# Performance work log

Measured on AMD Instinct MI355X. Metric: run time of the kernel, lower is better.

## Reference

```python
import jax, jax.numpy as jnp
import numpy as np

SIM_THRESHOLD = 0.9


def setup_inputs() -> dict:
    key = jax.random.key(0)
    k1, k2 = jax.random.split(key)
    # patches: b * c * num * ws * ws  (b=2, c=8, num=1024, ws=3) -> n = 16384
    patches = jax.random.normal(k1, (2, 8, 1024, 3, 3), dtype=jnp.float32)
    # db: m * ws * ws
    db = jax.random.normal(k2, (16384, 3, 3), dtype=jnp.float32)
    return {"patches": patches, "db": db}


def reference(patches, db):
    ws = patches.shape[-1]
    p = patches.reshape(-1, ws, ws)          # [n, ws, ws]
    n = p.shape[0]
    m = db.shape[0]
    pf = p.reshape(n, -1)                    # [n, ws*ws]
    df = db.reshape(m, -1)                   # [m, ws*ws]
    dot = pf @ df.T                          # [n, m], tiny K=ws*ws -> memory bound
    norm_n = jnp.linalg.norm(pf, axis=1, keepdims=True)   # [n, 1]
    norm_m = jnp.linalg.norm(df, axis=1, keepdims=True)   # [m, 1]
    cos = dot / (norm_n * norm_m.T)          # [n, m] cosine similarity
    # patch kept only if dissimilar to EVERY db entry
    mask = jnp.all(cos < SIM_THRESHOLD, axis=1)            # [n] bool
    # jit-friendly fixed-shape compaction: zero out rejected patches instead of
    # dropping rows (original does db = cat(db, patches[mask]))
    filtered = jnp.where(mask[:, None, None], p, jnp.zeros((), p.dtype))
    return jnp.concatenate([db.reshape(-1, ws, ws), filtered], axis=0)  # [m+n, ws, ws]
```

## Files before the change

### kernel.cpp

```cpp
#include <hip/hip_runtime.h>

#define NPATCH 16384
#define NDB    16384
#define WS9    9
#define KP     16
#define JCH    32
#define CHUNK  (NDB / JCH)
#define TILES  (CHUNK / 32)
#define BAND_LO 0.89998f
#define BAND_HI 0.90002f
#define COPY_BLOCKS 144

typedef short bf16x8 __attribute__((ext_vector_type(8)));
typedef float f32x16 __attribute__((ext_vector_type(16)));

#define MAX3(a,b,c) fmaxf(fmaxf((a),(b)),(c))

__device__ __forceinline__ float np_norm9(const float* v) {
#pragma clang fp contract(off)
    float q0 = v[0] * v[0], q1 = v[1] * v[1], q2 = v[2] * v[2], q3 = v[3] * v[3];
    float q4 = v[4] * v[4], q5 = v[5] * v[5], q6 = v[6] * v[6], q7 = v[7] * v[7];
    float q8 = v[8] * v[8];
    float s = ((q0 + q1) + (q2 + q3)) + ((q4 + q5) + (q6 + q7));
    s = s + q8;
    return sqrtf(s);
}

__device__ __forceinline__ unsigned short f2bf(float x) {
    unsigned u = __float_as_uint(x);
    return (unsigned short)((u + 0x7fffu + ((u >> 16) & 1u)) >> 16);
}
__device__ __forceinline__ float bf2f(unsigned short h) {
    return __uint_as_float(((unsigned)h) << 16);
}

__device__ __forceinline__ void stage_row(const float* __restrict__ src,
                                          unsigned short* dh, unsigned short* dl) {
    float v[WS9];
#pragma unroll
    for (int k = 0; k < WS9; k++) v[k] = src[k];
    float inv = 1.0f / np_norm9(v);
    unsigned short h[KP], l[KP];
#pragma unroll
    for (int k = 0; k < KP; k++) {
        float x = (k < WS9) ? v[k] * inv : 0.0f;
        h[k] = f2bf(x);
        l[k] = f2bf(x - bf2f(h[k]));
    }
    int hw[8], lw[8];
#pragma unroll
    for (int k = 0; k < 8; k++) {
        hw[k] = (int)h[2 * k] | ((int)h[2 * k + 1] << 16);
        lw[k] = (int)l[2 * k] | ((int)l[2 * k + 1] << 16);
    }
    ((int4*)dh)[0] = make_int4(hw[0], hw[1], hw[2], hw[3]);
    ((int4*)dh)[1] = make_int4(hw[4], hw[5], hw[6], hw[7]);
    ((int4*)dl)[0] = make_int4(lw[0], lw[1], lw[2], lw[3]);
    ((int4*)dl)[1] = make_int4(lw[4], lw[5], lw[6], lw[7]);
}

__global__ __launch_bounds__(256) void k_phase1(const float* __restrict__ patches,
                                                const float* __restrict__ db,
                                                float* __restrict__ partial) {
    __shared__ __align__(16) unsigned short s_dnh[CHUNK * KP];
    __shared__ __align__(16) unsigned short s_dnl[CHUNK * KP];
    __shared__ __align__(16) unsigned short s_pnh[256 * KP];
    __shared__ __align__(16) unsigned short s_pnl[256 * KP];

    int jbase = blockIdx.y * CHUNK;
    int ibase = blockIdx.x * 256;
#pragma unroll
    for (int rr = 0; rr < CHUNK / 256; rr++) {
        int r = rr * 256 + threadIdx.x;
        stage_row(db + (size_t)(jbase + r) * WS9, &s_dnh[r * KP], &s_dnl[r * KP]);
    }
    stage_row(patches + (size_t)(ibase + threadIdx.x) * WS9,
              &s_pnh[threadIdx.x * KP], &s_pnl[threadIdx.x * KP]);
    __syncthreads();

    int lane = threadIdx.x & 63;
    int wave = threadIdx.x >> 6;
    int col = lane & 31;
    int half = lane >> 5;
    int i0 = ibase + wave * 64;

    const bf16x8* Ph = (const bf16x8*)s_pnh;
    const bf16x8* Pl = (const bf16x8*)s_pnl;
    bf16x8 b_hi0 = Ph[(wave * 64 + col) * 2 + half];
    bf16x8 b_lo0 = Pl[(wave * 64 + col) * 2 + half];
    bf16x8 b_hi1 = Ph[(wave * 64 + 32 + col) * 2 + half];
    bf16x8 b_lo1 = Pl[(wave * 64 + 32 + col) * 2 + half];

    const bf16x8* Ah = (const bf16x8*)s_dnh;
    const bf16x8* Al = (const bf16x8*)s_dnl;

    f32x16 zc = {0.f,0.f,0.f,0.f,0.f,0.f,0.f,0.f,0.f,0.f,0.f,0.f,0.f,0.f,0.f,0.f};
    float rm0 = -3.0e38f, rm1 = -3.0e38f;

#pragma unroll 2
    for (int t = 0; t < TILES; ++t) {
        bf16x8 a_h = Ah[(t * 32 + col) * 2 + half];
        bf16x8 a_l = Al[(t * 32 + col) * 2 + half];
        f32x16 acc0 = __builtin_amdgcn_mfma_f32_32x32x16_bf16(a_h, b_hi0, zc, 0, 0, 0);
        acc0 = __builtin_amdgcn_mfma_f32_32x32x16_bf16(a_h, b_lo0, acc0, 0, 0, 0);
        acc0 = __builtin_amdgcn_mfma_f32_32x32x16_bf16(a_l, b_hi0, acc0, 0, 0, 0);
        f32x16 acc1 = __builtin_amdgcn_mfma_f32_32x32x16_bf16(a_h, b_hi1, zc, 0, 0, 0);
        acc1 = __builtin_amdgcn_mfma_f32_32x32x16_bf16(a_h, b_lo1, acc1, 0, 0, 0);
        acc1 = __builtin_amdgcn_mfma_f32_32x32x16_bf16(a_l, b_hi1, acc1, 0, 0, 0);
        {
            float u0 = MAX3(acc0[0],  acc0[1],  acc0[2]);
            float u1 = MAX3(acc0[3],  acc0[4],  acc0[5]);
            float u2 = MAX3(acc0[6],  acc0[7],  acc0[8]);
            float u3 = MAX3(acc0[9],  acc0[10], acc0[11]);
            float u4 = MAX3(acc0[12], acc0[13], acc0[14]);
            float u5 = MAX3(u0, u1, acc0[15]);
            float u6 = MAX3(u2, u3, u4);
            rm0 = MAX3(u5, u6, rm0);
        }
        {
            float u0 = MAX3(acc1[0],  acc1[1],  acc1[2]);
            float u1 = MAX3(acc1[3],  acc1[4],  acc1[5]);
            float u2 = MAX3(acc1[6],  acc1[7],  acc1[8]);
            float u3 = MAX3(acc1[9],  acc1[10], acc1[11]);
            float u4 = MAX3(acc1[12], acc1[13], acc1[14]);
            float u5 = MAX3(u0, u1, acc1[15]);
            float u6 = MAX3(u2, u3, u4);
            rm1 = MAX3(u5, u6, rm1);
        }
    }
    rm0 = fmaxf(rm0, __shfl_xor(rm0, 32, 64));
    rm1 = fmaxf(rm1, __shfl_xor(rm1, 32, 64));
    int ti = half ? (i0 + 32 + col) : (i0 + col);
    partial[(size_t)blockIdx.y * NPATCH + ti] = half ? rm1 : rm0;
}

__global__ __launch_bounds__(256) void k_finish(const float* __restrict__ patches,
                                                const float* __restrict__ db,
                                                const float* __restrict__ partial,
                                                float* __restrict__ out) {
    int b = blockIdx.x;
    if (b < COPY_BLOCKS) {
        int e = b * 256 + threadIdx.x;
        ((float4*)out)[e] = ((const float4*)db)[e];
        return;
    }
    __shared__ int s_bn;
    __shared__ int s_blist[256];
    __shared__ float sp[WS9];
    __shared__ float snp;
    __shared__ int shit;

    int tid = (int)threadIdx.x;
    int i = (b - COPY_BLOCKS) * 256 + tid;
    if (tid == 0) s_bn = 0;
    __syncthreads();

    float cosmax = partial[i];
#pragma unroll
    for (int c = 1; c < JCH; c++)
        cosmax = fmaxf(cosmax, partial[(size_t)c * NPATCH + i]);
    if (cosmax >= BAND_LO && cosmax < BAND_HI) {
        int idx = atomicAdd(&s_bn, 1);
        s_blist[idx] = i;
    } else {
        int hit = (cosmax >= BAND_HI) ? 1 : 0;
#pragma unroll
        for (int k = 0; k < WS9; k++)
            out[(size_t)(NDB + i) * WS9 + k] = hit ? 0.0f : patches[(size_t)i * WS9 + k];
    }
    __syncthreads();
    int nb = s_bn;

    for (int e = 0; e < nb; e++) {
        int bi = s_blist[e];
        if (tid == 0) {
            float p[WS9];
            for (int k = 0; k < WS9; k++) { p[k] = patches[(size_t)bi * WS9 + k]; sp[k] = p[k]; }
            snp = np_norm9(p);
            shit = 0;
        }
        __syncthreads();
        float p[WS9];
#pragma unroll
        for (int k = 0; k < WS9; k++) p[k] = sp[k];
        float npn = snp;
        int hit = 0;
        for (int j = tid; j < NDB; j += 256) {
            float d[WS9];
#pragma unroll
            for (int k = 0; k < WS9; k++) d[k] = db[(size_t)j * WS9 + k];
            float dot = 0.0f;
#pragma unroll
            for (int k = 0; k < WS9; k++) dot = fmaf(p[k], d[k], dot);
            float nd = np_norm9(d);
            float cs = dot / (npn * nd);
            if (!((double)cs < 0.9)) hit = 1;
        }
        if (hit) atomicOr(&shit, 1);
        __syncthreads();
        int m = shit;
        if (tid < WS9)
            out[(size_t)(NDB + bi) * WS9 + tid] = m ? 0.0f : sp[tid];
        __syncthreads();
    }
}

extern "C" void kernel_launch(void* const* d_in, const int* in_sizes, int n_in,
                              void* d_out, int out_size, void* d_ws, size_t ws_size,
                              hipStream_t stream) {
    const float* patches = (const float*)d_in[0];
    const float* db      = (const float*)d_in[1];
    float* out = (float*)d_out;

    float* partial = (float*)d_ws;

    k_phase1<<<dim3(NPATCH / 256, JCH), dim3(256), 0, stream>>>(patches, db, partial);
    k_finish<<<dim3(COPY_BLOCKS + NPATCH / 256), dim3(256), 0, stream>>>(
        patches, db, partial, out);
}
```

Baseline: 94.41 us.

## Loop each phase1 block over a db slice with double-buffered LDS staging

The grid's db dimension shrinks from 32 chunks to 8 slices. Each block now walks four 512-row chunks of its slice, prefetching the next chunk's db rows into registers and splitting them into the alternate LDS buffer while MFMAs run on the current one. Patch staging is amortized over more db rows, and k_finish has fewer partial maxima to reduce. The trade-off is a 512-block grid instead of 2048, which gives less parallelism and worse latency hiding, plus a per-chunk __syncthreads and more LDS per block.

```diff
diff --git a/kernel.cpp b/kernel.cpp
--- a/kernel.cpp
+++ b/kernel.cpp
@@ -4,8 +4,10 @@
 #define NDB    16384
 #define WS9    9
 #define KP     16
-#define JCH    32
-#define CHUNK  (NDB / JCH)
+#define NSL    8
+#define SLICE  (NDB / NSL)
+#define CHUNK  512
+#define NCH    (SLICE / CHUNK)
 #define TILES  (CHUNK / 32)
 #define BAND_LO 0.89998f
 #define BAND_HI 0.90002f
@@ -34,11 +36,8 @@
     return __uint_as_float(((unsigned)h) << 16);
 }
 
-__device__ __forceinline__ void stage_row(const float* __restrict__ src,
+__device__ __forceinline__ void split_row(const float* v,
                                           unsigned short* dh, unsigned short* dl) {
-    float v[WS9];
-#pragma unroll
-    for (int k = 0; k < WS9; k++) v[k] = src[k];
     float inv = 1.0f / np_norm9(v);
     unsigned short h[KP], l[KP];
 #pragma unroll
@@ -62,24 +61,36 @@
 __global__ __launch_bounds__(256) void k_phase1(const float* __restrict__ patches,
                                                 const float* __restrict__ db,
                                                 float* __restrict__ partial) {
-    __shared__ __align__(16) unsigned short s_dnh[CHUNK * KP];
-    __shared__ __align__(16) unsigned short s_dnl[CHUNK * KP];
     __shared__ __align__(16) unsigned short s_pnh[256 * KP];
     __shared__ __align__(16) unsigned short s_pnl[256 * KP];
-
-    int jbase = blockIdx.y * CHUNK;
+    __shared__ __align__(16) unsigned short s_dh[2][CHUNK * KP];
+    __shared__ __align__(16) unsigned short s_dl[2][CHUNK * KP];
+
+    int tid = (int)threadIdx.x;
+    int jbase = blockIdx.y * SLICE;
     int ibase = blockIdx.x * 256;
-#pragma unroll
-    for (int rr = 0; rr < CHUNK / 256; rr++) {
-        int r = rr * 256 + threadIdx.x;
-        stage_row(db + (size_t)(jbase + r) * WS9, &s_dnh[r * KP], &s_dnl[r * KP]);
-    }
-    stage_row(patches + (size_t)(ibase + threadIdx.x) * WS9,
-              &s_pnh[threadIdx.x * KP], &s_pnl[threadIdx.x * KP]);
+
+    {
+        float v[WS9];
+        const float* g = patches + (size_t)(ibase + tid) * WS9;
+#pragma unroll
+        for (int k = 0; k < WS9; k++) v[k] = g[k];
+        split_row(v, &s_pnh[tid * KP], &s_pnl[tid * KP]);
+    }
+
+    float va[WS9], vb[WS9];
+    {
+        const float* g0 = db + (size_t)(jbase + tid) * WS9;
+        const float* g1 = db + (size_t)(jbase + 256 + tid) * WS9;
+#pragma unroll
+        for (int k = 0; k < WS9; k++) { va[k] = g0[k]; vb[k] = g1[k]; }
+        split_row(va, &s_dh[0][tid * KP], &s_dl[0][tid * KP]);
+        split_row(vb, &s_dh[0][(256 + tid) * KP], &s_dl[0][(256 + tid) * KP]);
+    }
     __syncthreads();
 
-    int lane = threadIdx.x & 63;
-    int wave = threadIdx.x >> 6;
+    int lane = tid & 63;
+    int wave = tid >> 6;
     int col = lane & 31;
     int half = lane >> 5;
     int i0 = ibase + wave * 64;
@@ -91,43 +102,59 @@
     bf16x8 b_hi1 = Ph[(wave * 64 + 32 + col) * 2 + half];
     bf16x8 b_lo1 = Pl[(wave * 64 + 32 + col) * 2 + half];
 
-    const bf16x8* Ah = (const bf16x8*)s_dnh;
-    const bf16x8* Al = (const bf16x8*)s_dnl;
-
     f32x16 zc = {0.f,0.f,0.f,0.f,0.f,0.f,0.f,0.f,0.f,0.f,0.f,0.f,0.f,0.f,0.f,0.f};
     float rm0 = -3.0e38f, rm1 = -3.0e38f;
 
+    for (int c = 0; c < NCH; c++) {
+        int cur = c & 1;
+        if (c < NCH - 1) {
+            const float* p0 = db + (size_t)(jbase + (c + 1) * CHUNK + tid) * WS9;
+            const float* p1 = db + (size_t)(jbase + (c + 1) * CHUNK + 256 + tid) * WS9;
+#pragma unroll
+            for (int k = 0; k < WS9; k++) { va[k] = p0[k]; vb[k] = p1[k]; }
+        }
+
+        const bf16x8* Ah = (const bf16x8*)s_dh[cur];
+        const bf16x8* Al = (const bf16x8*)s_dl[cur];
 #pragma unroll 2
-    for (int t = 0; t < TILES; ++t) {
-        bf16x8 a_h = Ah[(t * 32 + col) * 2 + half];
-        bf16x8 a_l = Al[(t * 32 + col) * 2 + half];
-        f32x16 acc0 = __builtin_amdgcn_mfma_f32_32x32x16_bf16(a_h, b_hi0, zc, 0, 0, 0);
-        acc0 = __builtin_amdgcn_mfma_f32_32x32x16_bf16(a_h, b_lo0, acc0, 0, 0, 0);
-        acc0 = __builtin_amdgcn_mfma_f32_32x32x16_bf16(a_l, b_hi0, acc0, 0, 0, 0);
-        f32x16 acc1 = __builtin_amdgcn_mfma_f32_32x32x16_bf16(a_h, b_hi1, zc, 0, 0, 0);
-        acc1 = __builtin_amdgcn_mfma_f32_32x32x16_bf16(a_h, b_lo1, acc1, 0, 0, 0);
-        acc1 = __builtin_amdgcn_mfma_f32_32x32x16_bf16(a_l, b_hi1, acc1, 0, 0, 0);
-        {
-            float u0 = MAX3(acc0[0],  acc0[1],  acc0[2]);
-            float u1 = MAX3(acc0[3],  acc0[4],  acc0[5]);
-            float u2 = MAX3(acc0[6],  acc0[7],  acc0[8]);
-            float u3 = MAX3(acc0[9],  acc0[10], acc0[11]);
-            float u4 = MAX3(acc0[12], acc0[13], acc0[14]);
-            float u5 = MAX3(u0, u1, acc0[15]);
-            float u6 = MAX3(u2, u3, u4);
-            rm0 = MAX3(u5, u6, rm0);
-        }
-        {
-            float u0 = MAX3(acc1[0],  acc1[1],  acc1[2]);
-            float u1 = MAX3(acc1[3],  acc1[4],  acc1[5]);
-            float u2 = MAX3(acc1[6],  acc1[7],  acc1[8]);
-            float u3 = MAX3(acc1[9],  acc1[10], acc1[11]);
-            float u4 = MAX3(acc1[12], acc1[13], acc1[14]);
-            float u5 = MAX3(u0, u1, acc1[15]);
-            float u6 = MAX3(u2, u3, u4);
-            rm1 = MAX3(u5, u6, rm1);
-        }
-    }
+        for (int t = 0; t < TILES; ++t) {
+            bf16x8 a_h = Ah[(t * 32 + col) * 2 + half];
+            bf16x8 a_l = Al[(t * 32 + col) * 2 + half];
+            f32x16 acc0 = __builtin_amdgcn_mfma_f32_32x32x16_bf16(a_h, b_hi0, zc, 0, 0, 0);
+            acc0 = __builtin_amdgcn_mfma_f32_32x32x16_bf16(a_h, b_lo0, acc0, 0, 0, 0);
+            acc0 = __builtin_amdgcn_mfma_f32_32x32x16_bf16(a_l, b_hi0, acc0, 0, 0, 0);
+            f32x16 acc1 = __builtin_amdgcn_mfma_f32_32x32x16_bf16(a_h, b_hi1, zc, 0, 0, 0);
+            acc1 = __builtin_amdgcn_mfma_f32_32x32x16_bf16(a_h, b_lo1, acc1, 0, 0, 0);
+            acc1 = __builtin_amdgcn_mfma_f32_32x32x16_bf16(a_l, b_hi1, acc1, 0, 0, 0);
+            {
+                float u0 = MAX3(acc0[0],  acc0[1],  acc0[2]);
+                float u1 = MAX3(acc0[3],  acc0[4],  acc0[5]);
+                float u2 = MAX3(acc0[6],  acc0[7],  acc0[8]);
+                float u3 = MAX3(acc0[9],  acc0[10], acc0[11]);
+                float u4 = MAX3(acc0[12], acc0[13], acc0[14]);
+                float u5 = MAX3(u0, u1, acc0[15]);
+                float u6 = MAX3(u2, u3, u4);
+                rm0 = MAX3(u5, u6, rm0);
+            }
+            {
+                float u0 = MAX3(acc1[0],  acc1[1],  acc1[2]);
+                float u1 = MAX3(acc1[3],  acc1[4],  acc1[5]);
+                float u2 = MAX3(acc1[6],  acc1[7],  acc1[8]);
+                float u3 = MAX3(acc1[9],  acc1[10], acc1[11]);
+                float u4 = MAX3(acc1[12], acc1[13], acc1[14]);
+                float u5 = MAX3(u0, u1, acc1[15]);
+                float u6 = MAX3(u2, u3, u4);
+                rm1 = MAX3(u5, u6, rm1);
+            }
+        }
+
+        if (c < NCH - 1) {
+            split_row(va, &s_dh[cur ^ 1][tid * KP], &s_dl[cur ^ 1][tid * KP]);
+            split_row(vb, &s_dh[cur ^ 1][(256 + tid) * KP], &s_dl[cur ^ 1][(256 + tid) * KP]);
+        }
+        __syncthreads();
+    }
+
     rm0 = fmaxf(rm0, __shfl_xor(rm0, 32, 64));
     rm1 = fmaxf(rm1, __shfl_xor(rm1, 32, 64));
     int ti = half ? (i0 + 32 + col) : (i0 + col);
@@ -157,7 +184,7 @@
 
     float cosmax = partial[i];
 #pragma unroll
-    for (int c = 1; c < JCH; c++)
+    for (int c = 1; c < NSL; c++)
         cosmax = fmaxf(cosmax, partial[(size_t)c * NPATCH + i]);
     if (cosmax >= BAND_LO && cosmax < BAND_HI) {
         int idx = atomicAdd(&s_bn, 1);
@@ -214,7 +241,7 @@
 
     float* partial = (float*)d_ws;
 
-    k_phase1<<<dim3(NPATCH / 256, JCH), dim3(256), 0, stream>>>(patches, db, partial);
+    k_phase1<<<dim3(NPATCH / 256, NSL), dim3(256), 0, stream>>>(patches, db, partial);
     k_finish<<<dim3(COPY_BLOCKS + NPATCH / 256), dim3(256), 0, stream>>>(
         patches, db, partial, out);
 }
```

Measured after the change: 93.44 us. Within noise of the previous version (-1.0%).
